# Kernel tuning notes

Hardware: AMD Instinct MI355X
Metric: run time of the kernel (lower is better)

The kernel has to match this reference:

```python
import jax, jax.numpy as jnp
import numpy as np

B, S, D = 2, 2048, 1024
H = 16
DK = D // H
DFF = 4096
EPS = 1e-6


def rotate_half(x):
    x1, x2 = jnp.split(x, 2, axis=-1)
    return jnp.concatenate((-x2, x1), axis=-1)


def build_rope(dim, seq_len):
    inv_freq = 1.0 / (10000.0 ** (jnp.arange(0, dim, 2, dtype=jnp.float32) / dim))
    t = jnp.arange(seq_len, dtype=jnp.float32)
    freqs = jnp.einsum('i,j->ij', t, inv_freq)
    emb = jnp.concatenate((freqs, freqs), axis=-1)
    return jnp.cos(emb)[None, None], jnp.sin(emb)[None, None]  # [1,1,S,dk]


def rmsnorm(x, g):
    rms = jnp.sqrt(jnp.mean(x * x, axis=-1, keepdims=True) + EPS)
    return x / rms * g


def setup_inputs() -> dict:
    key = jax.random.key(0)
    ks = jax.random.split(key, 10)
    sc = 0.02
    x = jax.random.normal(ks[0], (B, S, D), dtype=jnp.float32)
    mask = jnp.tril(jnp.ones((S, S), dtype=jnp.int32))[None, None]  # causal [1,1,S,S]
    wq = jax.random.normal(ks[1], (D, D), dtype=jnp.float32) * sc
    wk = jax.random.normal(ks[2], (D, D), dtype=jnp.float32) * sc
    wv = jax.random.normal(ks[3], (D, D), dtype=jnp.float32) * sc
    wo = jax.random.normal(ks[4], (D, D), dtype=jnp.float32) * sc
    w1 = jax.random.normal(ks[5], (2 * DFF, D), dtype=jnp.float32) * sc
    w2 = jax.random.normal(ks[6], (D, DFF), dtype=jnp.float32) * sc
    g1 = jnp.ones((D,), dtype=jnp.float32)
    g2 = jnp.ones((D,), dtype=jnp.float32)
    return {"x": x, "mask": mask, "wq": wq, "wk": wk, "wv": wv, "wo": wo,
            "w1": w1, "w2": w2, "g1": g1, "g2": g2}


def decoder_block(x, mask, wq, wk, wv, wo, w1, w2, g1, g2):
    b, s, d = x.shape
    # --- self-attention sublayer ---
    h = rmsnorm(x, g1)
    q = (h @ wq.T).reshape(b, s, H, DK).transpose(0, 2, 1, 3)
    k = (h @ wk.T).reshape(b, s, H, DK).transpose(0, 2, 1, 3)
    v = (h @ wv.T).reshape(b, s, H, DK).transpose(0, 2, 1, 3)
    cos, sin = build_rope(DK, s)
    q = q * cos + rotate_half(q) * sin
    k = k * cos + rotate_half(k) * sin
    scores = jnp.einsum('bhqd,bhkd->bhqk', q, k) / jnp.sqrt(jnp.float32(DK))
    scores = jnp.where(mask == 0, jnp.float32(-1e9), scores)
    p = jax.nn.softmax(scores, axis=-1)
    ctx = jnp.einsum('bhqk,bhkd->bhqd', p, v)
    ctx = ctx.transpose(0, 2, 1, 3).reshape(b, s, d)
    x = x + ctx @ wo.T
    # --- SwiGLU FFN sublayer ---
    h2 = rmsnorm(x, g2)
    u = h2 @ w1.T  # [b,s,2*DFF]
    u1, u2 = jnp.split(u, 2, axis=-1)
    ffn = (u1 * jax.nn.silu(u2)) @ w2.T
    return x + ffn


def reference(x, mask, wq, wk, wv, wo, w1, w2, g1, g2):
    return decoder_block(x, mask, wq, wk, wv, wo, w1, w2, g1, g2)
```

## Files before the change

kernel.cpp:

```cpp
#include <hip/hip_runtime.h>
#include <hip/hip_bf16.h>

#define BB 2
#define SS 2048
#define DD 1024
#define NH 16
#define DKH 64
#define DFF 4096
#define MTOK (BB*SS)

typedef __hip_bfloat16 bf16;
typedef __attribute__((ext_vector_type(8))) short s16x8;
typedef __attribute__((ext_vector_type(4))) float f32x4;

__device__ __forceinline__ float bs2f(short s) {
    unsigned int u = ((unsigned int)(unsigned short)s) << 16;
    return __uint_as_float(u);
}
__device__ __forceinline__ float b2f(bf16 v) { return __bfloat162float(v); }
__device__ __forceinline__ bf16 f2b(float v) { return __float2bfloat16(v); }
__device__ __forceinline__ short f2bs(float v) {
    bf16 b = __float2bfloat16(v);
    return *(short*)&b;
}

__device__ __forceinline__ void load16(const bf16* g, bf16* l) {
    __builtin_amdgcn_global_load_lds((const __attribute__((address_space(1))) void*)g,
                                     (__attribute__((address_space(3))) void*)l,
                                     16, 0, 0);
}


__global__ void cvt_kernel(const float* __restrict__ src, bf16* __restrict__ dst) {
    const int i = blockIdx.x * blockDim.x + threadIdx.x;
    float4 v = ((const float4*)src)[i];
    short4 o;
    o.x = f2bs(v.x); o.y = f2bs(v.y); o.z = f2bs(v.z); o.w = f2bs(v.w);
    ((short4*)dst)[i] = o;
}

__global__ void cvt4_kernel(const float* __restrict__ s0, const float* __restrict__ s1,
                            const float* __restrict__ s2, const float* __restrict__ s3,
                            bf16* __restrict__ dst) {
    const int z = blockIdx.z;
    const float* src = (z == 0) ? s0 : (z == 1) ? s1 : (z == 2) ? s2 : s3;
    const int i = blockIdx.x * blockDim.x + threadIdx.x;
    float4 v = ((const float4*)src)[i];
    short4 o;
    o.x = f2bs(v.x); o.y = f2bs(v.y); o.z = f2bs(v.z); o.w = f2bs(v.w);
    ((short4*)(dst + (size_t)z * DD * DD))[i] = o;
}

__global__ void rmsnorm_kernel(const float* __restrict__ x, const float* __restrict__ g,
                               bf16* __restrict__ out) {
    const int row = blockIdx.x;
    const int tid = threadIdx.x;
    float4 xv = ((const float4*)(x + (size_t)row * DD))[tid];
    float ss = xv.x*xv.x + xv.y*xv.y + xv.z*xv.z + xv.w*xv.w;
    #pragma unroll
    for (int off = 32; off > 0; off >>= 1) ss += __shfl_down(ss, off);
    __shared__ float red[4];
    const int wv = tid >> 6, lane = tid & 63;
    if (lane == 0) red[wv] = ss;
    __syncthreads();
    const float tot = red[0] + red[1] + red[2] + red[3];
    const float inv = rsqrtf(tot * (1.0f / DD) + 1e-6f);
    float4 gv = ((const float4*)g)[tid];
    short4 o;
    o.x = f2bs(xv.x * inv * gv.x);
    o.y = f2bs(xv.y * inv * gv.y);
    o.z = f2bs(xv.z * inv * gv.z);
    o.w = f2bs(xv.w * inv * gv.w);
    ((short4*)(out + (size_t)row * DD))[tid] = o;
}

__global__ __launch_bounds__(256) void gemm_qkv(const bf16* __restrict__ A,
                                                const bf16* __restrict__ Wbase,
                                                bf16* __restrict__ Obase) {
    __shared__ bf16 As[128 * 32];
    __shared__ bf16 Bs[128 * 32];
    const int tid = threadIdx.x, lane = tid & 63, wv = tid >> 6;
    const int col = lane & 15, quad = lane >> 4;
    const int wm = wv >> 1, wn = wv & 1;
    const int m0 = blockIdx.y * 128;
    const int n0 = blockIdx.x * 128;
    const bf16* W = Wbase + (size_t)blockIdx.z * DD * DD;
    bf16* C = Obase + (size_t)blockIdx.z * MTOK * DD;

    const int srow = tid >> 2;
    const int scol = (((tid & 3) ^ (srow & 3))) * 8;
    const bf16* Ag = A + (size_t)(m0 + srow) * DD + scol;
    const bf16* Wg = W + (size_t)(n0 + srow) * DD + scol;
    bf16* Asl = As + tid * 8;
    bf16* Bsl = Bs + tid * 8;
    const size_t half = (size_t)64 * DD;
    const int rg = (quad ^ (col & 3)) * 8;

    f32x4 acc[4][4] = {};
    for (int k0 = 0; k0 < DD; k0 += 32) {
        __syncthreads();
        load16(Ag + k0,        Asl);
        load16(Ag + half + k0, Asl + 2048);
        load16(Wg + k0,        Bsl);
        load16(Wg + half + k0, Bsl + 2048);
        __syncthreads();
        s16x8 af[4], bfr[4];
        #pragma unroll
        for (int t = 0; t < 4; t++) {
            af[t]  = *(const s16x8*)(As + (wm * 64 + t * 16 + col) * 32 + rg);
            bfr[t] = *(const s16x8*)(Bs + (wn * 64 + t * 16 + col) * 32 + rg);
        }
        #pragma unroll
        for (int tm = 0; tm < 4; tm++)
            #pragma unroll
            for (int tn = 0; tn < 4; tn++)
                acc[tm][tn] = __builtin_amdgcn_mfma_f32_16x16x32_bf16(af[tm], bfr[tn], acc[tm][tn], 0, 0, 0);
    }
    #pragma unroll
    for (int tm = 0; tm < 4; tm++)
        #pragma unroll
        for (int tn = 0; tn < 4; tn++)
            #pragma unroll
            for (int r = 0; r < 4; r++) {
                const int rr = m0 + wm * 64 + tm * 16 + quad * 4 + r;
                const int cc = n0 + wn * 64 + tn * 16 + col;
                C[(size_t)rr * DD + cc] = f2b(acc[tm][tn][r]);
            }
}

__global__ __launch_bounds__(256) void gemm128_atomic(const bf16* __restrict__ A,
                                                      const bf16* __restrict__ W,
                                                      float* C, int N, int K, int KC) {
    __shared__ bf16 As[128 * 32];
    __shared__ bf16 Bs[128 * 32];
    const int tid = threadIdx.x, lane = tid & 63, wv = tid >> 6;
    const int col = lane & 15, quad = lane >> 4;
    const int wm = wv >> 1, wn = wv & 1;
    const int m0 = blockIdx.y * 128;
    const int n0 = blockIdx.x * 128;
    const int koff = blockIdx.z * KC;

    const int srow = tid >> 2;
    const int scol = (((tid & 3) ^ (srow & 3))) * 8;
    const bf16* Ag = A + (size_t)(m0 + srow) * K + scol;
    const bf16* Wg = W + (size_t)(n0 + srow) * K + scol;
    bf16* Asl = As + tid * 8;
    bf16* Bsl = Bs + tid * 8;
    const size_t half = (size_t)64 * K;
    const int rg = (quad ^ (col & 3)) * 8;

    f32x4 acc[4][4] = {};
    for (int k0 = koff; k0 < koff + KC; k0 += 32) {
        __syncthreads();
        load16(Ag + k0,        Asl);
        load16(Ag + half + k0, Asl + 2048);
        load16(Wg + k0,        Bsl);
        load16(Wg + half + k0, Bsl + 2048);
        __syncthreads();
        s16x8 af[4], bfr[4];
        #pragma unroll
        for (int t = 0; t < 4; t++) {
            af[t]  = *(const s16x8*)(As + (wm * 64 + t * 16 + col) * 32 + rg);
            bfr[t] = *(const s16x8*)(Bs + (wn * 64 + t * 16 + col) * 32 + rg);
        }
        #pragma unroll
        for (int tm = 0; tm < 4; tm++)
            #pragma unroll
            for (int tn = 0; tn < 4; tn++)
                acc[tm][tn] = __builtin_amdgcn_mfma_f32_16x16x32_bf16(af[tm], bfr[tn], acc[tm][tn], 0, 0, 0);
    }
    #pragma unroll
    for (int tm = 0; tm < 4; tm++)
        #pragma unroll
        for (int tn = 0; tn < 4; tn++)
            #pragma unroll
            for (int r = 0; r < 4; r++) {
                const int rr = m0 + wm * 64 + tm * 16 + quad * 4 + r;
                const int cc = n0 + wn * 64 + tn * 16 + col;
                atomicAdd(&C[(size_t)rr * N + cc], acc[tm][tn][r]);
            }
}

__global__ __launch_bounds__(256) void gemm64n_f32res(const bf16* __restrict__ A,
                                                      const bf16* __restrict__ W,
                                                      const float* res, float* C,
                                                      int M, int N, int K) {
    __shared__ bf16 As[128 * 32];
    __shared__ bf16 Bs[64 * 32];
    const int tid = threadIdx.x, lane = tid & 63, wv = tid >> 6;
    const int col = lane & 15, quad = lane >> 4;
    const int wm = wv >> 1, wn = wv & 1;
    const int m0 = blockIdx.y * 128;
    const int n0 = blockIdx.x * 64;

    const int srow = tid >> 2;
    const int scol = (((tid & 3) ^ (srow & 3))) * 8;
    const bf16* Ag = A + (size_t)(m0 + srow) * K + scol;
    const bf16* Wg = W + (size_t)(n0 + srow) * K + scol;
    bf16* Asl = As + tid * 8;
    bf16* Bsl = Bs + tid * 8;
    const size_t half = (size_t)64 * K;
    const int rg = (quad ^ (col & 3)) * 8;

    f32x4 acc[4][2] = {};
    for (int k0 = 0; k0 < K; k0 += 32) {
        __syncthreads();
        load16(Ag + k0,        Asl);
        load16(Ag + half + k0, Asl + 2048);
        load16(Wg + k0,        Bsl);
        __syncthreads();
        s16x8 af[4], bfr[2];
        #pragma unroll
        for (int t = 0; t < 4; t++)
            af[t] = *(const s16x8*)(As + (wm * 64 + t * 16 + col) * 32 + rg);
        #pragma unroll
        for (int t = 0; t < 2; t++)
            bfr[t] = *(const s16x8*)(Bs + (wn * 32 + t * 16 + col) * 32 + rg);
        #pragma unroll
        for (int tm = 0; tm < 4; tm++)
            #pragma unroll
            for (int tn = 0; tn < 2; tn++)
                acc[tm][tn] = __builtin_amdgcn_mfma_f32_16x16x32_bf16(af[tm], bfr[tn], acc[tm][tn], 0, 0, 0);
    }
    #pragma unroll
    for (int tm = 0; tm < 4; tm++)
        #pragma unroll
        for (int tn = 0; tn < 2; tn++)
            #pragma unroll
            for (int r = 0; r < 4; r++) {
                const int rr = m0 + wm * 64 + tm * 16 + quad * 4 + r;
                const int cc = n0 + wn * 32 + tn * 16 + col;
                C[(size_t)rr * N + cc] = acc[tm][tn][r] + res[(size_t)rr * N + cc];
            }
}

__device__ __forceinline__ void stage_sw(const bf16* Ag, const bf16* Wg0, const bf16* Wg1,
                                         bf16* Asl, bf16* Bsl, int k0) {
    load16(Ag + k0,                        Asl);
    load16(Ag + k0 + 32,                   Asl + 8192);
    load16(Ag + (size_t)128 * DD + k0,     Asl + 4096);
    load16(Ag + (size_t)128 * DD + k0 + 32, Asl + 8192 + 4096);
    load16(Wg0 + k0,                       Bsl);
    load16(Wg0 + k0 + 32,                  Bsl + 8192);
    load16(Wg1 + k0,                       Bsl + 4096);
    load16(Wg1 + k0 + 32,                  Bsl + 8192 + 4096);
}

__device__ __forceinline__ void compute_sw(const bf16* Ab, const bf16* Bb,
                                           f32x4 (*acc)[4],
                                           int wm, int wn, int col, int quad) {
    const int rg = (quad ^ (col & 3)) * 8;
    #pragma unroll
    for (int kk = 0; kk < 2; kk++) {
        const bf16* Ap = Ab + kk * 8192;
        const bf16* Bp = Bb + kk * 8192;
        s16x8 af[8], bfr[4];
        #pragma unroll
        for (int t = 0; t < 8; t++)
            af[t] = *(const s16x8*)(Ap + (wm * 128 + t * 16 + col) * 32 + rg);
        #pragma unroll
        for (int t = 0; t < 4; t++)
            bfr[t] = *(const s16x8*)(Bp + (wn * 64 + t * 16 + col) * 32 + rg);
        #pragma unroll
        for (int tm = 0; tm < 8; tm++)
            #pragma unroll
            for (int tn = 0; tn < 4; tn++)
                acc[tm][tn] = __builtin_amdgcn_mfma_f32_16x16x32_bf16(af[tm], bfr[tn], acc[tm][tn], 0, 0, 0);
    }
}

__global__ __launch_bounds__(512, 2) void gemm256_swiglu(const bf16* __restrict__ A,
                                                         const bf16* __restrict__ W,
                                                         bf16* __restrict__ G,
                                                         int ybase) {
    __shared__ bf16 As[2][2][256 * 32];
    __shared__ bf16 Bs[2][2][256 * 32];
    const int tid = threadIdx.x, lane = tid & 63, wv = tid >> 6;
    const int col = lane & 15, quad = lane >> 4;
    const int wm = wv >> 2, wn = wv & 3;
    const int m0 = (blockIdx.y + ybase) * 256;
    const int n0 = blockIdx.x * 128;

    const int srow = tid >> 2;
    const int scol = ((tid & 3) ^ (srow & 3)) * 8;
    const bf16* Ag = A + (size_t)(m0 + srow) * DD + scol;
    const int r0 = srow, r1 = srow + 128;
    const int wr0 = n0 + ((r0 >> 6) << 5) + (r0 & 31) + (((r0 >> 5) & 1) ? DFF : 0);
    const int wr1 = n0 + ((r1 >> 6) << 5) + (r1 & 31) + (((r1 >> 5) & 1) ? DFF : 0);
    const bf16* Wg0 = W + (size_t)wr0 * DD + scol;
    const bf16* Wg1 = W + (size_t)wr1 * DD + scol;
    bf16* Asl = &As[0][0][0] + tid * 8;
    bf16* Bsl = &Bs[0][0][0] + tid * 8;
    const int bufoff = 2 * 8192;

    f32x4 acc[8][4] = {};

    stage_sw(Ag, Wg0, Wg1, Asl, Bsl, 0);
    __syncthreads();
    int buf = 0;
    for (int t = 0; t < 15; t++) {
        stage_sw(Ag, Wg0, Wg1, Asl + (buf ^ 1) * bufoff, Bsl + (buf ^ 1) * bufoff,
                 (t + 1) * 64);
        compute_sw(&As[buf][0][0], &Bs[buf][0][0], acc, wm, wn, col, quad);
        __syncthreads();
        buf ^= 1;
    }
    compute_sw(&As[buf][0][0], &Bs[buf][0][0], acc, wm, wn, col, quad);

    #pragma unroll
    for (int tm = 0; tm < 8; tm++)
        #pragma unroll
        for (int tn = 0; tn < 2; tn++)
            #pragma unroll
            for (int r = 0; r < 4; r++) {
                const int rr = m0 + wm * 128 + tm * 16 + quad * 4 + r;
                const int cc = n0 + wn * 32 + tn * 16 + col;
                const float u1 = acc[tm][tn][r];
                const float u2 = acc[tm][tn + 2][r];
                const float sig = 1.0f / (1.0f + __expf(-u2));
                G[(size_t)rr * DFF + cc] = f2b(u1 * u2 * sig);
            }
}

__global__ void rope_table_kernel(float2* __restrict__ tbl) {
    const int i = blockIdx.x * blockDim.x + threadIdx.x;
    const int d = i & 31, s = i >> 5;
    const float invf = powf(10000.0f, -(float)d * (1.0f / 32.0f));
    float sn, cs;
    sincosf((float)s * invf, &sn, &cs);
    tbl[i] = make_float2(cs, sn);
}

__global__ __launch_bounds__(256) void rope_vec_kernel(bf16* __restrict__ q,
                                                       bf16* __restrict__ k,
                                                       const float2* __restrict__ tbl) {
    const int tid = threadIdx.x, lane = tid & 63, wv = tid >> 6;
    const int row = blockIdx.x * 4 + wv;
    const int s = row & (SS - 1);
    const int h = lane >> 2, dp = (lane & 3) * 8;
    const size_t base = (size_t)row * DD + h * DKH + dp;
    float2 cs[8];
    #pragma unroll
    for (int j = 0; j < 8; j++) cs[j] = tbl[s * 32 + dp + j];
    s16x8 qlo = *(const s16x8*)(q + base), qhi = *(const s16x8*)(q + base + 32);
    s16x8 klo = *(const s16x8*)(k + base), khi = *(const s16x8*)(k + base + 32);
    s16x8 qlo2, qhi2, klo2, khi2;
    #pragma unroll
    for (int j = 0; j < 8; j++) {
        float x1 = bs2f(qlo[j]), x2 = bs2f(qhi[j]);
        qlo2[j] = f2bs(x1 * cs[j].x - x2 * cs[j].y);
        qhi2[j] = f2bs(x2 * cs[j].x + x1 * cs[j].y);
        x1 = bs2f(klo[j]); x2 = bs2f(khi[j]);
        klo2[j] = f2bs(x1 * cs[j].x - x2 * cs[j].y);
        khi2[j] = f2bs(x2 * cs[j].x + x1 * cs[j].y);
    }
    *(s16x8*)(q + base) = qlo2;
    *(s16x8*)(q + base + 32) = qhi2;
    *(s16x8*)(k + base) = klo2;
    *(s16x8*)(k + base + 32) = khi2;
}

__global__ __launch_bounds__(256) void vt_transpose(const bf16* __restrict__ v,
                                                    bf16* __restrict__ vt) {
    __shared__ short tile[64][72];
    const int s0 = blockIdx.x * 64;
    const int bh = blockIdx.y;
    const int b = bh >> 4, h = bh & 15;
    const bf16* src = v + (size_t)b * SS * DD + h * DKH;
    #pragma unroll
    for (int it = 0; it < 2; it++) {
        const int sl = (threadIdx.x >> 3) + it * 32;
        const int dp = (threadIdx.x & 7) * 8;
        s16x8 val = *(const s16x8*)(src + (size_t)(s0 + sl) * DD + dp);
        *(s16x8*)&tile[sl][dp] = val;
    }
    __syncthreads();
    bf16* dst = vt + (size_t)bh * DKH * SS;
    #pragma unroll
    for (int it = 0; it < 2; it++) {
        const int dk = (threadIdx.x >> 3) + it * 32;
        const int sp = (threadIdx.x & 7) * 8;
        s16x8 o;
        #pragma unroll
        for (int j = 0; j < 8; j++) o[j] = tile[sp + j][dk];
        *(s16x8*)(dst + (size_t)dk * SS + s0 + sp) = o;
    }
}

__device__ __forceinline__ void stage_kv(const bf16* kbase, const bf16* vtbase,
                                         bf16* Kd, bf16* Vd, int kt0, int tid) {
    const int row0 = tid >> 3;
    const int gl = tid & 7;
    #pragma unroll
    for (int r = 0; r < 2; r++) {
        const int row = row0 + r * 32;
        const int g = (gl ^ (row & 7)) * 8;
        load16(kbase + (size_t)(kt0 + row) * DD + g, Kd + tid * 8 + r * 2048);
        load16(vtbase + (size_t)row * SS + kt0 + g,  Vd + tid * 8 + r * 2048);
    }
}

__device__ __forceinline__ void attn_step(const bf16* Ks, const bf16* Vs,
                                          short (*pl)[72],
                                          s16x8 qf0, s16x8 qf1,
                                          f32x4* cacc, float* lacc,
                                          int col, int quad, int kt0, int q0w,
                                          bool need_mask) {
    f32x4 s4[4] = {};
    #pragma unroll
    for (int t = 0; t < 4; t++) {
        const int key = 16 * t + col;
        const int g0 = (quad ^ (key & 7)) * 8;
        s16x8 b0 = *(const s16x8*)(Ks + key * 64 + g0);
        s16x8 b1 = *(const s16x8*)(Ks + key * 64 + (g0 ^ 32));
        s4[t] = __builtin_amdgcn_mfma_f32_16x16x32_bf16(qf0, b0, s4[t], 0, 0, 0);
        s4[t] = __builtin_amdgcn_mfma_f32_16x16x32_bf16(qf1, b1, s4[t], 0, 0, 0);
    }
    #pragma unroll
    for (int t = 0; t < 4; t++)
        #pragma unroll
        for (int r = 0; r < 4; r++) {
            float sv = s4[t][r] * 0.125f;
            if (need_mask) {
                const int key = kt0 + 16 * t + col;
                const int qq  = q0w + quad * 4 + r;
                if (key > qq) sv = -1.0e30f;
            }
            const float p = __expf(sv);
            s4[t][r] = p;
            lacc[r] += p;
        }
    #pragma unroll
    for (int t = 0; t < 4; t++)
        #pragma unroll
        for (int r = 0; r < 4; r++)
            pl[quad * 4 + r][col + 16 * t] = f2bs(s4[t][r]);
    s16x8 pf0 = *(const s16x8*)&pl[col][quad * 8];
    s16x8 pf1 = *(const s16x8*)&pl[col][32 + quad * 8];
    #pragma unroll
    for (int tn = 0; tn < 4; tn++) {
        const int dk = 16 * tn + col;
        const int g0 = (quad ^ (dk & 7)) * 8;
        s16x8 b0 = *(const s16x8*)(Vs + dk * 64 + g0);
        s16x8 b1 = *(const s16x8*)(Vs + dk * 64 + (g0 ^ 32));
        cacc[tn] = __builtin_amdgcn_mfma_f32_16x16x32_bf16(pf0, b0, cacc[tn], 0, 0, 0);
        cacc[tn] = __builtin_amdgcn_mfma_f32_16x16x32_bf16(pf1, b1, cacc[tn], 0, 0, 0);
    }
}

__device__ __forceinline__ void attn_step2(const bf16* Ks, const bf16* Vs,
                                           short (*pl)[72],
                                           s16x8 qA0, s16x8 qA1,
                                           s16x8 qB0, s16x8 qB1,
                                           f32x4* caccA, f32x4* caccB,
                                           float* lA, float* lB,
                                           int col, int quad, int kt0, int q0A,
                                           bool maskA) {
    f32x4 sA[4] = {}, sB[4] = {};
    #pragma unroll
    for (int t = 0; t < 4; t++) {
        const int key = 16 * t + col;
        const int g0 = (quad ^ (key & 7)) * 8;
        s16x8 b0 = *(const s16x8*)(Ks + key * 64 + g0);
        s16x8 b1 = *(const s16x8*)(Ks + key * 64 + (g0 ^ 32));
        sA[t] = __builtin_amdgcn_mfma_f32_16x16x32_bf16(qA0, b0, sA[t], 0, 0, 0);
        sA[t] = __builtin_amdgcn_mfma_f32_16x16x32_bf16(qA1, b1, sA[t], 0, 0, 0);
        sB[t] = __builtin_amdgcn_mfma_f32_16x16x32_bf16(qB0, b0, sB[t], 0, 0, 0);
        sB[t] = __builtin_amdgcn_mfma_f32_16x16x32_bf16(qB1, b1, sB[t], 0, 0, 0);
    }
    #pragma unroll
    for (int t = 0; t < 4; t++)
        #pragma unroll
        for (int r = 0; r < 4; r++) {
            float svA = sA[t][r] * 0.125f;
            if (maskA) {
                const int key = kt0 + 16 * t + col;
                const int qq  = q0A + quad * 4 + r;
                if (key > qq) svA = -1.0e30f;
            }
            const float pA = __expf(svA);
            sA[t][r] = pA;
            lA[r] += pA;
            const float pB = __expf(sB[t][r] * 0.125f);
            sB[t][r] = pB;
            lB[r] += pB;
        }
    #pragma unroll
    for (int t = 0; t < 4; t++)
        #pragma unroll
        for (int r = 0; r < 4; r++)
            pl[quad * 4 + r][col + 16 * t] = f2bs(sA[t][r]);
    s16x8 pA0 = *(const s16x8*)&pl[col][quad * 8];
    s16x8 pA1 = *(const s16x8*)&pl[col][32 + quad * 8];
    #pragma unroll
    for (int t = 0; t < 4; t++)
        #pragma unroll
        for (int r = 0; r < 4; r++)
            pl[quad * 4 + r][col + 16 * t] = f2bs(sB[t][r]);
    s16x8 pB0 = *(const s16x8*)&pl[col][quad * 8];
    s16x8 pB1 = *(const s16x8*)&pl[col][32 + quad * 8];
    #pragma unroll
    for (int tn = 0; tn < 4; tn++) {
        const int dk = 16 * tn + col;
        const int g0 = (quad ^ (dk & 7)) * 8;
        s16x8 b0 = *(const s16x8*)(Vs + dk * 64 + g0);
        s16x8 b1 = *(const s16x8*)(Vs + dk * 64 + (g0 ^ 32));
        caccA[tn] = __builtin_amdgcn_mfma_f32_16x16x32_bf16(pA0, b0, caccA[tn], 0, 0, 0);
        caccA[tn] = __builtin_amdgcn_mfma_f32_16x16x32_bf16(pA1, b1, caccA[tn], 0, 0, 0);
        caccB[tn] = __builtin_amdgcn_mfma_f32_16x16x32_bf16(pB0, b0, caccB[tn], 0, 0, 0);
        caccB[tn] = __builtin_amdgcn_mfma_f32_16x16x32_bf16(pB1, b1, caccB[tn], 0, 0, 0);
    }
}

__global__ __launch_bounds__(256) void attn_mfma2(const bf16* __restrict__ q,
                                                  const bf16* __restrict__ k,
                                                  const bf16* __restrict__ vt,
                                                  bf16* __restrict__ ctx) {
    __shared__ bf16 Ks[2][64 * 64];
    __shared__ bf16 Vs[2][64 * 64];
    __shared__ short plds[4][16][72];
    const int tid = threadIdx.x, lane = tid & 63, wv = tid >> 6;
    const int col = lane & 15, quad = lane >> 4;
    const int bh = blockIdx.y;
    const int b = bh >> 4, h = bh & 15;
    const int tA = blockIdx.x;
    const int tB = 31 - tA;
    const int q0A = tA * 64 + wv * 16;
    const int q0B = tB * 64 + wv * 16;

    const bf16* kbase  = k  + (size_t)b * SS * DD + h * DKH;
    const bf16* vtbase = vt + (size_t)bh * DKH * SS;

    const bf16* qrA = q + (size_t)(b * SS + q0A + col) * DD + h * DKH + quad * 8;
    const bf16* qrB = q + (size_t)(b * SS + q0B + col) * DD + h * DKH + quad * 8;
    s16x8 qfA0 = *(const s16x8*)(qrA);
    s16x8 qfA1 = *(const s16x8*)(qrA + 32);
    s16x8 qfB0 = *(const s16x8*)(qrB);
    s16x8 qfB1 = *(const s16x8*)(qrB + 32);

    f32x4 caccA[4] = {}, caccB[4] = {};
    float lA[4] = {}, lB[4] = {};

    const int last = tB;
    stage_kv(kbase, vtbase, Ks[0], Vs[0], 0, tid);
    int buf = 0;
    for (int kt = 0; kt <= last; kt++) {
        __syncthreads();
        if (kt < last)
            stage_kv(kbase, vtbase, Ks[buf ^ 1], Vs[buf ^ 1], (kt + 1) * 64, tid);
        const bf16* Kc = Ks[buf];
        const bf16* Vc = Vs[buf];
        if (kt <= tA)
            attn_step2(Kc, Vc, plds[wv], qfA0, qfA1, qfB0, qfB1,
                       caccA, caccB, lA, lB, col, quad, kt * 64, q0A, kt == tA);
        else
            attn_step(Kc, Vc, plds[wv], qfB0, qfB1, caccB, lB,
                      col, quad, kt * 64, q0B, kt == tB);
        buf ^= 1;
    }
    #pragma unroll
    for (int r = 0; r < 4; r++) {
        #pragma unroll
        for (int off = 1; off < 16; off <<= 1) {
            lA[r] += __shfl_xor(lA[r], off);
            lB[r] += __shfl_xor(lB[r], off);
        }
    }
    #pragma unroll
    for (int tn = 0; tn < 4; tn++)
        #pragma unroll
        for (int r = 0; r < 4; r++) {
            const size_t tokA = (size_t)(b * SS + q0A + quad * 4 + r);
            ctx[tokA * DD + h * DKH + 16 * tn + col] = f2b(caccA[tn][r] / lA[r]);
            const size_t tokB = (size_t)(b * SS + q0B + quad * 4 + r);
            ctx[tokB * DD + h * DKH + 16 * tn + col] = f2b(caccB[tn][r] / lB[r]);
        }
}

extern "C" void kernel_launch(void* const* d_in, const int* in_sizes, int n_in,
                              void* d_out, int out_size, void* d_ws, size_t ws_size,
                              hipStream_t stream) {
    const float* x  = (const float*)d_in[0];
    const float* wq = (const float*)d_in[2];
    const float* wk = (const float*)d_in[3];
    const float* wv = (const float*)d_in[4];
    const float* wo = (const float*)d_in[5];
    const float* w1 = (const float*)d_in[6];
    const float* w2 = (const float*)d_in[7];
    const float* g1 = (const float*)d_in[8];
    const float* g2 = (const float*)d_in[9];
    float* out = (float*)d_out;
    char* ws = (char*)d_ws;

    const size_t MB = 1024 * 1024;
    bf16* hb   = (bf16*)(ws + 0 * MB);
    bf16* qb   = (bf16*)(ws + 8 * MB);
    bf16* kb   = (bf16*)(ws + 16 * MB);
    bf16* vb   = (bf16*)(ws + 24 * MB);
    bf16* ctxb = hb;
    bf16* h2b  = hb;
    bf16* gb   = qb;
    bf16* wqb  = (bf16*)(ws + 32 * MB);
    bf16* wob  = wqb + (size_t)3 * DD * DD;
    bf16* vtb  = (bf16*)(ws + 40 * MB);
    float2* rtb = (float2*)(ws + 48 * MB);
    bf16* w1b  = (bf16*)(ws + 40 * MB);
    bf16* w2b  = (bf16*)(ws + 56 * MB);

    cvt4_kernel<<<dim3((DD * DD / 4) / 256, 1, 4), 256, 0, stream>>>(
        wq, wk, wv, wo, wqb);

    rope_table_kernel<<<(SS * 32) / 256, 256, 0, stream>>>(rtb);

    rmsnorm_kernel<<<MTOK, 256, 0, stream>>>(x, g1, hb);
    gemm_qkv<<<dim3(DD / 128, MTOK / 128, 3), 256, 0, stream>>>(hb, wqb, qb);

    vt_transpose<<<dim3(SS / 64, BB * NH), 256, 0, stream>>>(vb, vtb);
    rope_vec_kernel<<<MTOK / 4, 256, 0, stream>>>(qb, kb, rtb);

    attn_mfma2<<<dim3(16, BB * NH), 256, 0, stream>>>(qb, kb, vtb, ctxb);

    gemm64n_f32res<<<dim3(DD / 64, MTOK / 128), 256, 0, stream>>>(
        ctxb, wob, x, out, MTOK, DD, DD);
    rmsnorm_kernel<<<MTOK, 256, 0, stream>>>(out, g2, h2b);

    cvt_kernel<<<(2 * DFF * DD / 4) / 256, 256, 0, stream>>>(w1, w1b);
    cvt_kernel<<<(DD * DFF / 4) / 256, 256, 0, stream>>>(w2, w2b);

    gemm256_swiglu<<<dim3(DFF / 128, 8), 512, 0, stream>>>(h2b, w1b, gb, 0);
    gemm256_swiglu<<<dim3(DFF / 128, 8), 512, 0, stream>>>(h2b, w1b, gb, 8);
    gemm128_atomic<<<dim3(DD / 128, MTOK / 128, 2), 256, 0, stream>>>(
        gb, w2b, out, DD, DFF, DFF / 2);
}
```

Baseline: 440.9 us.

## Replace atomic split-K down-projection with 4-way partial buffers plus reduction

The final FFN down-projection GEMM moves from a 2-way split-K with float atomicAdd into the output to a 4-way split-K. Each split writes plain stores into its own fp32 partial buffer, and a separate kernel then sums the four partials into the output. The new GEMM also stages 64 K-elements per sync in two LDS buffers, which halves the number of barriers. This is meant to remove atomic contention and raise grid parallelism, at the cost of 64MB of extra partial traffic and one more launch. It falls back to the atomic path if the workspace is too small.

```diff
diff --git a/kernel.cpp b/kernel.cpp
--- a/kernel.cpp
+++ b/kernel.cpp
@@ -179,6 +179,84 @@
                 const int cc = n0 + wn * 64 + tn * 16 + col;
                 atomicAdd(&C[(size_t)rr * N + cc], acc[tm][tn][r]);
             }
+}
+
+__global__ __launch_bounds__(256) void gemm128_part(const bf16* __restrict__ A,
+                                                    const bf16* __restrict__ W,
+                                                    float* __restrict__ P,
+                                                    int N, int K, int KC) {
+    __shared__ bf16 As[2][128 * 32];
+    __shared__ bf16 Bs[2][128 * 32];
+    const int tid = threadIdx.x, lane = tid & 63, wv = tid >> 6;
+    const int col = lane & 15, quad = lane >> 4;
+    const int wm = wv >> 1, wn = wv & 1;
+    const int m0 = blockIdx.y * 128;
+    const int n0 = blockIdx.x * 128;
+    const int koff = blockIdx.z * KC;
+    float* Pz = P + (size_t)blockIdx.z * MTOK * N;
+
+    const int srow = tid >> 2;
+    const int scol = (((tid & 3) ^ (srow & 3))) * 8;
+    const bf16* Ag = A + (size_t)(m0 + srow) * K + scol;
+    const bf16* Wg = W + (size_t)(n0 + srow) * K + scol;
+    const size_t half = (size_t)64 * K;
+    const int rg = (quad ^ (col & 3)) * 8;
+
+    f32x4 acc[4][4] = {};
+    for (int k0 = koff; k0 < koff + KC; k0 += 64) {
+        __syncthreads();
+        load16(Ag + k0,             As[0] + tid * 8);
+        load16(Ag + half + k0,      As[0] + tid * 8 + 2048);
+        load16(Ag + k0 + 32,        As[1] + tid * 8);
+        load16(Ag + half + k0 + 32, As[1] + tid * 8 + 2048);
+        load16(Wg + k0,             Bs[0] + tid * 8);
+        load16(Wg + half + k0,      Bs[0] + tid * 8 + 2048);
+        load16(Wg + k0 + 32,        Bs[1] + tid * 8);
+        load16(Wg + half + k0 + 32, Bs[1] + tid * 8 + 2048);
+        __syncthreads();
+        #pragma unroll
+        for (int kk = 0; kk < 2; kk++) {
+            s16x8 af[4], bfr[4];
+            #pragma unroll
+            for (int t = 0; t < 4; t++) {
+                af[t]  = *(const s16x8*)(As[kk] + (wm * 64 + t * 16 + col) * 32 + rg);
+                bfr[t] = *(const s16x8*)(Bs[kk] + (wn * 64 + t * 16 + col) * 32 + rg);
+            }
+            #pragma unroll
+            for (int tm = 0; tm < 4; tm++)
+                #pragma unroll
+                for (int tn = 0; tn < 4; tn++)
+                    acc[tm][tn] = __builtin_amdgcn_mfma_f32_16x16x32_bf16(af[tm], bfr[tn], acc[tm][tn], 0, 0, 0);
+        }
+    }
+    #pragma unroll
+    for (int tm = 0; tm < 4; tm++)
+        #pragma unroll
+        for (int tn = 0; tn < 4; tn++)
+            #pragma unroll
+            for (int r = 0; r < 4; r++) {
+                const int rr = m0 + wm * 64 + tm * 16 + quad * 4 + r;
+                const int cc = n0 + wn * 64 + tn * 16 + col;
+                Pz[(size_t)rr * N + cc] = acc[tm][tn][r];
+            }
+}
+
+__global__ __launch_bounds__(256) void reduce4_kernel(const float4* __restrict__ P,
+                                                      float4* __restrict__ out) {
+    const size_t n4 = (size_t)MTOK * DD / 4;
+    for (size_t i = (size_t)blockIdx.x * blockDim.x + threadIdx.x; i < n4;
+         i += (size_t)gridDim.x * blockDim.x) {
+        float4 a = out[i];
+        const float4 p0 = P[i];
+        const float4 p1 = P[i + n4];
+        const float4 p2 = P[i + 2 * n4];
+        const float4 p3 = P[i + 3 * n4];
+        a.x += p0.x + p1.x + p2.x + p3.x;
+        a.y += p0.y + p1.y + p2.y + p3.y;
+        a.z += p0.z + p1.z + p2.z + p3.z;
+        a.w += p0.w + p1.w + p2.w + p3.w;
+        out[i] = a;
+    }
 }
 
 __global__ __launch_bounds__(256) void gemm64n_f32res(const bf16* __restrict__ A,
@@ -606,6 +684,8 @@
     float2* rtb = (float2*)(ws + 48 * MB);
     bf16* w1b  = (bf16*)(ws + 40 * MB);
     bf16* w2b  = (bf16*)(ws + 56 * MB);
+    float* pb  = (float*)(ws + 64 * MB);
+    const size_t ws_needed = 64 * MB + (size_t)4 * MTOK * DD * sizeof(float);
 
     cvt4_kernel<<<dim3((DD * DD / 4) / 256, 1, 4), 256, 0, stream>>>(
         wq, wk, wv, wo, wqb);
@@ -629,6 +709,13 @@
 
     gemm256_swiglu<<<dim3(DFF / 128, 8), 512, 0, stream>>>(h2b, w1b, gb, 0);
     gemm256_swiglu<<<dim3(DFF / 128, 8), 512, 0, stream>>>(h2b, w1b, gb, 8);
-    gemm128_atomic<<<dim3(DD / 128, MTOK / 128, 2), 256, 0, stream>>>(
-        gb, w2b, out, DD, DFF, DFF / 2);
-}
+
+    if (ws_size >= ws_needed) {
+        gemm128_part<<<dim3(DD / 128, MTOK / 128, 4), 256, 0, stream>>>(
+            gb, w2b, pb, DD, DFF, DFF / 4);
+        reduce4_kernel<<<2048, 256, 0, stream>>>((const float4*)pb, (float4*)out);
+    } else {
+        gemm128_atomic<<<dim3(DD / 128, MTOK / 128, 2), 256, 0, stream>>>(
+            gb, w2b, out, DD, DFF, DFF / 2);
+    }
+}
```

After: 442.1 us. About the same (+0.3%).
